# Performance work log

Hardware: AMD Instinct MI355X
Metric: run time of the kernel (lower is better)

The kernel has to match this reference:

```python
import jax, jax.numpy as jnp
import numpy as np

N_NODES = 100000
N_EDGES = 1600000
IN_DIM = 128
OUT_DIM = 128


def setup_inputs() -> dict:
    key = jax.random.key(0)
    k1, k2, k3, k4, k5 = jax.random.split(key, 5)
    features = jax.random.normal(k1, (N_NODES, IN_DIM), dtype=jnp.float32)
    # Xavier-uniform-ish init for the dense transform weight
    limit = float(np.sqrt(6.0 / (IN_DIM + OUT_DIM)))
    weight = jax.random.uniform(k2, (IN_DIM, OUT_DIM), dtype=jnp.float32,
                                minval=-limit, maxval=limit)
    bias = jnp.zeros((OUT_DIM,), dtype=jnp.float32)
    # Sparse adjacency in COO form: edge i contributes
    # edge_weight[i] * support[src[i]] into output row dst[i].
    edge_weight = jax.random.uniform(k3, (N_EDGES,), dtype=jnp.float32)
    src = jax.random.randint(k4, (N_EDGES,), 0, N_NODES)
    dst = jax.random.randint(k5, (N_EDGES,), 0, N_NODES)
    return {"features": features, "weight": weight, "bias": bias,
            "edge_weight": edge_weight, "src": src, "dst": dst}


def reference(features, weight, bias, edge_weight, src, dst):
    # support = X @ W  (dense GEMM: [N, in] x [in, out])
    support = features @ weight
    # output = A @ support, with A sparse in COO form -> gather + scatter-add
    msgs = support[src] * edge_weight[:, None]          # [E, out]
    out = jax.ops.segment_sum(msgs, dst, num_segments=features.shape[0])
    return out + bias
```

## Files before the change

kernel.cpp:

```cpp
#include <hip/hip_runtime.h>
#include <hip/hip_bf16.h>

#define DIM 128
#define EPB 4096
#define SRC_BITS 17
#define SRC_MASK 0x1FFFF
#define TMAX 8

typedef short short8 __attribute__((ext_vector_type(8)));
typedef float f32x4 __attribute__((ext_vector_type(4)));

static __device__ __forceinline__ unsigned short f2bf(float f) {
    unsigned u = __builtin_bit_cast(unsigned, f);
    unsigned r = (u + 0x7fffu + ((u >> 16) & 1u)) >> 16;
    return (unsigned short)r;
}

__global__ __launch_bounds__(256) void gemm_xw_mfma(const float* __restrict__ X,
                                                    const float* __restrict__ W,
                                                    unsigned short* __restrict__ S2,
                                                    int n_nodes) {
    __shared__ unsigned short wlds[DIM * DIM];

    for (int idx = threadIdx.x; idx < DIM * DIM; idx += 256) {
        const int k = idx >> 7;
        const int n = idx & 127;
        wlds[n * DIM + (k ^ ((n & 7) << 3))] = f2bf(W[idx]);
    }
    __syncthreads();

    const int wave = threadIdx.x >> 6;
    const int lane = threadIdx.x & 63;
    const int row_base = blockIdx.x * 64 + wave * 16;
    const int mrow = lane & 15;
    const int kq = lane >> 4;
    const int kq8 = kq * 8;

    int rr = row_base + mrow;
    if (rr >= n_nodes) rr = n_nodes - 1;
    const float4* Xr = (const float4*)(X + (size_t)rr * DIM);

    short8 a[4];
#pragma unroll
    for (int s = 0; s < 4; ++s) {
        const float4 v0 = Xr[s * 8 + kq * 2];
        const float4 v1 = Xr[s * 8 + kq * 2 + 1];
        short8 av;
        av[0] = f2bf(v0.x); av[1] = f2bf(v0.y); av[2] = f2bf(v0.z); av[3] = f2bf(v0.w);
        av[4] = f2bf(v1.x); av[5] = f2bf(v1.y); av[6] = f2bf(v1.z); av[7] = f2bf(v1.w);
        a[s] = av;
    }

    f32x4 acc[8];
#pragma unroll
    for (int c = 0; c < 8; ++c) acc[c] = (f32x4){0.f, 0.f, 0.f, 0.f};

    const int swz = (lane & 7) << 3;
#pragma unroll
    for (int s = 0; s < 4; ++s) {
        const int k0 = s * 32 + kq8;
#pragma unroll
        for (int c = 0; c < 8; ++c) {
            const int n = c * 16 + mrow;
            const short8 bv = *(const short8*)(&wlds[n * DIM + (k0 ^ swz)]);
            acc[c] = __builtin_amdgcn_mfma_f32_16x16x32_bf16(a[s], bv, acc[c], 0, 0, 0);
        }
    }

#pragma unroll
    for (int reg = 0; reg < 4; ++reg) {
        const int g_r = row_base + kq * 4 + reg;
        if (g_r < n_nodes) {
            unsigned short* orow = S2 + (size_t)g_r * DIM + mrow;
#pragma unroll
            for (int c = 0; c < 8; ++c) orow[c * 16] = f2bf(acc[c][reg]);
        }
    }
}

__global__ __launch_bounds__(1024) void partA_hist(const int* __restrict__ dst,
                                                   int* __restrict__ cnt,
                                                   int n_edges, int nchunks, int nbkt) {
    __shared__ int lc[512];
    const int blk = blockIdx.x;
    for (int i = threadIdx.x; i < 512; i += 1024) lc[i] = 0;
    __syncthreads();
    const int base = blk * EPB;
#pragma unroll
    for (int u = 0; u < 4; ++u) {
        const int e = base + u * 1024 + threadIdx.x;
        if (e < n_edges) atomicAdd(&lc[dst[e] >> 8], 1);
    }
    __syncthreads();
    for (int b = threadIdx.x; b < nbkt; b += 1024) cnt[b * nchunks + blk] = lc[b];
}

#define SCAN_B 1024
__global__ __launch_bounds__(SCAN_B) void scan_block(const int* __restrict__ in,
                                                     int* __restrict__ outv,
                                                     int* __restrict__ bsum,
                                                     int n) {
    __shared__ int lds[SCAN_B];
    const int i = blockIdx.x * SCAN_B + threadIdx.x;
    int v = (i < n) ? in[i] : 0;
    const int own = v;
    lds[threadIdx.x] = v;
    __syncthreads();
#pragma unroll
    for (int off = 1; off < SCAN_B; off <<= 1) {
        int t = (threadIdx.x >= off) ? lds[threadIdx.x - off] : 0;
        __syncthreads();
        lds[threadIdx.x] += t;
        __syncthreads();
    }
    if (i < n) outv[i] = lds[threadIdx.x] - own;
    if (threadIdx.x == SCAN_B - 1) bsum[blockIdx.x] = lds[threadIdx.x];
}

__global__ __launch_bounds__(SCAN_B) void scan_tops(int* __restrict__ bsum, int nblocks) {
    __shared__ int lds[SCAN_B];
    int v = (threadIdx.x < nblocks) ? bsum[threadIdx.x] : 0;
    const int own = v;
    lds[threadIdx.x] = v;
    __syncthreads();
#pragma unroll
    for (int off = 1; off < SCAN_B; off <<= 1) {
        int t = (threadIdx.x >= off) ? lds[threadIdx.x - off] : 0;
        __syncthreads();
        lds[threadIdx.x] += t;
        __syncthreads();
    }
    if (threadIdx.x < nblocks) bsum[threadIdx.x] = lds[threadIdx.x] - own;
}

__global__ __launch_bounds__(SCAN_B) void scan_fix(int* __restrict__ outv,
                                                   const int* __restrict__ bsum,
                                                   int n) {
    const int i = blockIdx.x * SCAN_B + threadIdx.x;
    if (i < n) outv[i] += bsum[blockIdx.x];
}

__global__ __launch_bounds__(1024) void partB_scatter(const int* __restrict__ dst,
                                                      const int* __restrict__ src,
                                                      const float* __restrict__ ew,
                                                      const int* __restrict__ cb,
                                                      int2* __restrict__ part_sw,
                                                      int n_edges, int nchunks) {
    __shared__ int lc[512];
    const int blk = blockIdx.x;
    for (int i = threadIdx.x; i < 512; i += 1024) lc[i] = 0;
    __syncthreads();
    const int base = blk * EPB;
#pragma unroll
    for (int u = 0; u < 4; ++u) {
        const int e = base + u * 1024 + threadIdx.x;
        if (e < n_edges) {
            const int d = dst[e];
            const int bin = d >> 8;
            const int r = atomicAdd(&lc[bin], 1);
            const int pos = cb[bin * nchunks + blk] + r;
            part_sw[pos] = make_int2(src[e] | ((d & 255) << SRC_BITS),
                                     __float_as_int(ew[e]));
        }
    }
}

__global__ __launch_bounds__(1024) void partC_csr(const int2* __restrict__ part_sw,
                                                  const int* __restrict__ cb,
                                                  int* __restrict__ offsets,
                                                  int2* __restrict__ edge_sw,
                                                  int n_nodes, int n_edges,
                                                  int nchunks, int nbkt) {
    __shared__ int lcnt[256];
    __shared__ int loff[256];
    const int b = blockIdx.x;
    const int bstart = cb[b * nchunks];
    const int bend = (b + 1 < nbkt) ? cb[(b + 1) * nchunks] : n_edges;
    const int bcount = bend - bstart;

    if (threadIdx.x < 256) lcnt[threadIdx.x] = 0;
    __syncthreads();

    int2 sw_r[TMAX];
    int rk_r[TMAX];
    const int ntile = (bcount + 1023) >> 10;
#pragma unroll
    for (int t = 0; t < TMAX; ++t) {
        if (t < ntile) {
            const int i = t * 1024 + threadIdx.x;
            if (i < bcount) {
                const int2 v = part_sw[bstart + i];
                sw_r[t] = v;
                rk_r[t] = atomicAdd(&lcnt[(v.x >> SRC_BITS) & 255], 1);
            }
        }
    }
    __syncthreads();

    if (threadIdx.x < 256) loff[threadIdx.x] = lcnt[threadIdx.x];
    __syncthreads();
#pragma unroll
    for (int off = 1; off < 256; off <<= 1) {
        int t_ = 0;
        if (threadIdx.x < 256 && threadIdx.x >= off) t_ = loff[threadIdx.x - off];
        __syncthreads();
        if (threadIdx.x < 256) loff[threadIdx.x] += t_;
        __syncthreads();
    }
    int ex = 0;
    if (threadIdx.x < 256 && threadIdx.x > 0) ex = loff[threadIdx.x - 1];
    __syncthreads();
    if (threadIdx.x < 256) loff[threadIdx.x] = ex;
    __syncthreads();

    const int nb0 = b << 8;
    if (threadIdx.x < 256 && nb0 + threadIdx.x < n_nodes)
        offsets[nb0 + threadIdx.x] = bstart + loff[threadIdx.x];

#pragma unroll
    for (int t = 0; t < TMAX; ++t) {
        if (t < ntile) {
            const int i = t * 1024 + threadIdx.x;
            if (i < bcount) {
                const int ld = (sw_r[t].x >> SRC_BITS) & 255;
                edge_sw[bstart + loff[ld] + rk_r[t]] =
                    make_int2(sw_r[t].x & SRC_MASK, sw_r[t].y);
            }
        }
    }
}

__global__ __launch_bounds__(256) void gcn_reduce(const __hip_bfloat162* __restrict__ S2,
                                                  const int2* __restrict__ edge_sw,
                                                  const int* __restrict__ offsets,
                                                  const float* __restrict__ bias,
                                                  float* __restrict__ out,
                                                  int n_nodes, int n_edges) {
    const int node = blockIdx.x * 4 + (threadIdx.x >> 6);
    if (node >= n_nodes) return;
    const int lane = threadIdx.x & 63;

    const int start = offsets[node];
    const int end = (node + 1 < n_nodes) ? offsets[node + 1] : n_edges;

    float2 acc = ((const float2*)bias)[lane];

    for (int base = start; base < end; base += 64) {
        const int cnt = min(64, end - base);
        int2 meta = make_int2(0, 0);
        if (lane < cnt) meta = edge_sw[base + lane];

        int i = 0;
        for (; i + 8 <= cnt; i += 8) {
            float2 sv[8];
#pragma unroll
            for (int u = 0; u < 8; ++u) {
                const int s = __shfl(meta.x, i + u, 64);
                sv[u] = __bfloat1622float2(S2[(size_t)s * (DIM / 2) + lane]);
            }
#pragma unroll
            for (int u = 0; u < 8; ++u) {
                const float w = __int_as_float(__shfl(meta.y, i + u, 64));
                acc.x = fmaf(w, sv[u].x, acc.x);
                acc.y = fmaf(w, sv[u].y, acc.y);
            }
        }
        for (; i < cnt; ++i) {
            const int s = __shfl(meta.x, i, 64);
            const float w = __int_as_float(__shfl(meta.y, i, 64));
            const float2 sv = __bfloat1622float2(S2[(size_t)s * (DIM / 2) + lane]);
            acc.x = fmaf(w, sv.x, acc.x);
            acc.y = fmaf(w, sv.y, acc.y);
        }
    }

    ((float2*)(out + (size_t)node * DIM))[lane] = acc;
}

extern "C" void kernel_launch(void* const* d_in, const int* in_sizes, int n_in,
                              void* d_out, int out_size, void* d_ws, size_t ws_size,
                              hipStream_t stream) {
    const float* X    = (const float*)d_in[0];
    const float* W    = (const float*)d_in[1];
    const float* bias = (const float*)d_in[2];
    const float* ew   = (const float*)d_in[3];
    const int*   src  = (const int*)d_in[4];
    const int*   dst  = (const int*)d_in[5];
    float* out = (float*)d_out;

    const int n_nodes = in_sizes[0] / DIM;
    const int n_edges = in_sizes[3];

    const int nbkt = (n_nodes + 255) >> 8;
    const int nchunks = (n_edges + EPB - 1) / EPB;
    const int N2 = nbkt * nchunks;

    char* ws = (char*)d_ws;
    __hip_bfloat162* S2 = (__hip_bfloat162*)ws;
    char* p = ws + (size_t)n_nodes * (DIM / 2) * 4;
    int* cnt = (int*)p;             p += (size_t)N2 * 4;
    int* cb  = (int*)p;             p += (size_t)N2 * 4;
    int* bsum = (int*)p;            p += SCAN_B * 4;
    int* offsets = (int*)p;         p += (size_t)n_nodes * 4;
    int2* part_sw = (int2*)p;       p += (size_t)n_edges * 8;
    int2* edge_sw = (int2*)p;

    gemm_xw_mfma<<<(n_nodes + 63) / 64, 256, 0, stream>>>(X, W,
                                                          (unsigned short*)S2, n_nodes);

    partA_hist<<<nchunks, 1024, 0, stream>>>(dst, cnt, n_edges, nchunks, nbkt);

    const int nblocks = (N2 + SCAN_B - 1) / SCAN_B;
    scan_block<<<nblocks, SCAN_B, 0, stream>>>(cnt, cb, bsum, N2);
    scan_tops<<<1, SCAN_B, 0, stream>>>(bsum, nblocks);
    scan_fix<<<nblocks, SCAN_B, 0, stream>>>(cb, bsum, N2);

    partB_scatter<<<nchunks, 1024, 0, stream>>>(dst, src, ew, cb, part_sw,
                                                n_edges, nchunks);
    partC_csr<<<nbkt, 1024, 0, stream>>>(part_sw, cb, offsets, edge_sw,
                                         n_nodes, n_edges, nchunks, nbkt);

    gcn_reduce<<<(n_nodes + 3) / 4, 256, 0, stream>>>(S2, edge_sw, offsets,
                                                      bias, out, n_nodes, n_edges);
}
```

Baseline: 136.7 us.

## Fuse dst histogram into GEMM launch and enlarge edge chunk size

The separate histogram kernel is merged into the GEMM launch as extra blocks that reuse the weight LDS buffer for bucket counters, so the histogram runs alongside the GEMM and one launch is removed. The edges per chunk grow from 4096 to 16384, which shrinks the count/offset matrix and the scan work, and leaves fewer, longer-running blocks in the histogram and scatter passes. Fewer chunks mean less parallelism in partB_scatter and more LDS atomic contention per block.

```diff
diff --git a/kernel.cpp b/kernel.cpp
--- a/kernel.cpp
+++ b/kernel.cpp
@@ -2,7 +2,7 @@
 #include <hip/hip_bf16.h>
 
 #define DIM 128
-#define EPB 4096
+#define EPB 16384
 #define SRC_BITS 17
 #define SRC_MASK 0x1FFFF
 #define TMAX 8
@@ -16,11 +16,30 @@
     return (unsigned short)r;
 }
 
-__global__ __launch_bounds__(256) void gemm_xw_mfma(const float* __restrict__ X,
-                                                    const float* __restrict__ W,
-                                                    unsigned short* __restrict__ S2,
-                                                    int n_nodes) {
+__global__ __launch_bounds__(256) void gemm_hist(const float* __restrict__ X,
+                                                 const float* __restrict__ W,
+                                                 unsigned short* __restrict__ S2,
+                                                 const int* __restrict__ dst,
+                                                 int* __restrict__ cnt,
+                                                 int n_nodes, int n_edges,
+                                                 int nchunks, int nbkt, int gemmB) {
     __shared__ unsigned short wlds[DIM * DIM];
+
+    if (blockIdx.x >= gemmB) {
+        int* lc = (int*)wlds;
+        const int blk = blockIdx.x - gemmB;
+        for (int i = threadIdx.x; i < nbkt; i += 256) lc[i] = 0;
+        __syncthreads();
+        const int base = blk * EPB;
+#pragma unroll 4
+        for (int u = 0; u < EPB / 256; ++u) {
+            const int e = base + u * 256 + threadIdx.x;
+            if (e < n_edges) atomicAdd(&lc[dst[e] >> 8], 1);
+        }
+        __syncthreads();
+        for (int b = threadIdx.x; b < nbkt; b += 256) cnt[b * nchunks + blk] = lc[b];
+        return;
+    }
 
     for (int idx = threadIdx.x; idx < DIM * DIM; idx += 256) {
         const int k = idx >> 7;
@@ -76,23 +95,6 @@
             for (int c = 0; c < 8; ++c) orow[c * 16] = f2bf(acc[c][reg]);
         }
     }
-}
-
-__global__ __launch_bounds__(1024) void partA_hist(const int* __restrict__ dst,
-                                                   int* __restrict__ cnt,
-                                                   int n_edges, int nchunks, int nbkt) {
-    __shared__ int lc[512];
-    const int blk = blockIdx.x;
-    for (int i = threadIdx.x; i < 512; i += 1024) lc[i] = 0;
-    __syncthreads();
-    const int base = blk * EPB;
-#pragma unroll
-    for (int u = 0; u < 4; ++u) {
-        const int e = base + u * 1024 + threadIdx.x;
-        if (e < n_edges) atomicAdd(&lc[dst[e] >> 8], 1);
-    }
-    __syncthreads();
-    for (int b = threadIdx.x; b < nbkt; b += 1024) cnt[b * nchunks + blk] = lc[b];
 }
 
 #define SCAN_B 1024
@@ -152,7 +154,7 @@
     __syncthreads();
     const int base = blk * EPB;
 #pragma unroll
-    for (int u = 0; u < 4; ++u) {
+    for (int u = 0; u < EPB / 1024; ++u) {
         const int e = base + u * 1024 + threadIdx.x;
         if (e < n_edges) {
             const int d = dst[e];
@@ -294,10 +296,11 @@
     const int nbkt = (n_nodes + 255) >> 8;
     const int nchunks = (n_edges + EPB - 1) / EPB;
     const int N2 = nbkt * nchunks;
+    const int gemmB = (n_nodes + 63) / 64;
 
     char* ws = (char*)d_ws;
-    __hip_bfloat162* S2 = (__hip_bfloat162*)ws;
-    char* p = ws + (size_t)n_nodes * (DIM / 2) * 4;
+    unsigned short* S2 = (unsigned short*)ws;
+    char* p = ws + (size_t)n_nodes * DIM * 2;
     int* cnt = (int*)p;             p += (size_t)N2 * 4;
     int* cb  = (int*)p;             p += (size_t)N2 * 4;
     int* bsum = (int*)p;            p += SCAN_B * 4;
@@ -305,10 +308,9 @@
     int2* part_sw = (int2*)p;       p += (size_t)n_edges * 8;
     int2* edge_sw = (int2*)p;
 
-    gemm_xw_mfma<<<(n_nodes + 63) / 64, 256, 0, stream>>>(X, W,
-                                                          (unsigned short*)S2, n_nodes);
-
-    partA_hist<<<nchunks, 1024, 0, stream>>>(dst, cnt, n_edges, nchunks, nbkt);
+    gemm_hist<<<gemmB + nchunks, 256, 0, stream>>>(X, W, S2, dst, cnt,
+                                                   n_nodes, n_edges,
+                                                   nchunks, nbkt, gemmB);
 
     const int nblocks = (N2 + SCAN_B - 1) / SCAN_B;
     scan_block<<<nblocks, SCAN_B, 0, stream>>>(cnt, cb, bsum, N2);
@@ -320,6 +322,7 @@
     partC_csr<<<nbkt, 1024, 0, stream>>>(part_sw, cb, offsets, edge_sw,
                                          n_nodes, n_edges, nchunks, nbkt);
 
-    gcn_reduce<<<(n_nodes + 3) / 4, 256, 0, stream>>>(S2, edge_sw, offsets,
+    gcn_reduce<<<(n_nodes + 3) / 4, 256, 0, stream>>>((const __hip_bfloat162*)S2,
+                                                      edge_sw, offsets,
                                                       bias, out, n_nodes, n_edges);
 }
```

Result: slower. 156.7 us (+14.6%).
